# Optimization experiments

Hardware: AMD Instinct MI355X
Metric: run time of the kernel (lower is better)

Reference implementation:

```python
import jax, jax.numpy as jnp
import numpy as np

USER_NUM = 100000   # number of users
ITEM_NUM = 50000    # number of items
HIDDEN = 64         # embedding dim
B = 16384           # batch size
K = 50              # neighbors per item


def setup_inputs() -> dict:
    key = jax.random.key(0)
    ks = jax.random.split(key, 8)
    user = jax.random.randint(ks[0], (B,), 0, USER_NUM, dtype=jnp.int32)
    # item ids are offset by USER_NUM into the shared embedding table
    pos = USER_NUM + jax.random.randint(ks[1], (B,), 0, ITEM_NUM, dtype=jnp.int32)
    neg = USER_NUM + jax.random.randint(ks[2], (B,), 0, ITEM_NUM, dtype=jnp.int32)
    pos_beta = jax.random.uniform(ks[3], (B,), dtype=jnp.float32)
    neg_beta = jax.random.uniform(ks[4], (B,), dtype=jnp.float32)
    weights = jax.random.uniform(ks[5], (ITEM_NUM, K), dtype=jnp.float32)
    neighbor = jax.random.randint(ks[6], (ITEM_NUM, K), 0, USER_NUM, dtype=jnp.int32)
    embs = 0.02 * jax.random.normal(ks[7], (USER_NUM + ITEM_NUM, HIDDEN), dtype=jnp.float32)
    return {"user": user, "pos": pos, "neg": neg, "pos_beta": pos_beta,
            "neg_beta": neg_beta, "weights": weights, "neighbor": neighbor,
            "embs": embs}


def reference(user, pos, neg, pos_beta, neg_beta, weights, neighbor, embs):
    user_emb = embs[user]                      # [B, D]
    pos_emb = embs[pos]                        # [B, D]
    neg_emb = embs[neg]                        # [B, D]
    item_idx = pos - USER_NUM                  # [B]
    pos_neighbor = neighbor[item_idx]          # [B, K] user ids
    pos_weight = weights[item_idx]             # [B, K]
    pos_neighbor_emb = embs[pos_neighbor]      # [B, K, D]

    pos_logits = jnp.einsum('id,id->i', user_emb, pos_emb)            # [B]
    neg_logits = jnp.einsum('id,id->i', user_emb, neg_emb)            # [B]
    pos_nb_logits = jnp.einsum('id,ikd->ik', user_emb, pos_neighbor_emb)  # [B, K]

    # -log(sigmoid(x)) == -log_sigmoid(x), numerically stable
    log_sig_pos = jax.nn.log_sigmoid(pos_logits)
    log_sig_negneg = jax.nn.log_sigmoid(-neg_logits)

    LI = jnp.sum(-jax.nn.log_sigmoid(pos_nb_logits) * pos_weight)
    LO = -jnp.sum(log_sig_pos) - jnp.sum(log_sig_negneg)
    LC = -jnp.sum(log_sig_pos * pos_beta) - jnp.sum(log_sig_negneg * neg_beta)
    return LC + LO + 2.5 * LI
```

## Files before the change

kernel.cpp:

```cpp
#include <hip/hip_runtime.h>

#define USER_NUM 100000
#define ITEM_NUM 50000
#define HIDDEN   64
#define BATCH    16384
#define KNB      50

__device__ __forceinline__ float log_sigmoid(float x) {
    return fminf(x, 0.0f) - __logf(1.0f + __expf(-fabsf(x)));
}

__device__ __forceinline__ float dot4(float4 a, float4 b) {
    return a.x * b.x + a.y * b.y + a.z * b.z + a.w * b.w;
}

__device__ __forceinline__ float red16(float v) {
    v += __shfl_xor(v, 1);
    v += __shfl_xor(v, 2);
    v += __shfl_xor(v, 4);
    v += __shfl_xor(v, 8);
    return v;
}

__global__ __launch_bounds__(256) void ultragcn_main(
    const int*   __restrict__ user,
    const int*   __restrict__ pos,
    const int*   __restrict__ neg,
    const float* __restrict__ pos_beta,
    const float* __restrict__ neg_beta,
    const float* __restrict__ weights,
    const int*   __restrict__ neighbor,
    const float* __restrict__ embs,
    float*       __restrict__ partial)
{
    const int tid  = threadIdx.x;
    const int wave = tid >> 6;
    const int lane = tid & 63;
    const int i    = blockIdx.x * 4 + wave;

    const int g  = lane >> 4;
    const int gl = lane & 15;

    const int u = user[i];
    const int p = pos[i];
    const int n = neg[i];

    const float4* embs4 = (const float4*)embs;

    const float4 u4 = embs4[(long long)u * 16 + gl];
    const float4 p4 = embs4[(long long)p * 16 + gl];
    const float4 n4 = embs4[(long long)n * 16 + gl];

    const float pos_logit = red16(dot4(u4, p4));
    const float neg_logit = red16(dot4(u4, n4));

    const int item = p - USER_NUM;

    int   nbv = 0;
    float wv  = 0.0f;
    if (lane < KNB) {
        nbv = neighbor[item * KNB + lane];
        wv  = weights[item * KNB + lane];
    }

    float li = 0.0f;
#pragma unroll
    for (int t = 0; t < 13; ++t) {
        const int   k  = 4 * t + g;
        const int   nb = __shfl(nbv, k);
        const float w  = __shfl(wv,  k);
        const float4 e4 = embs4[(long long)nb * 16 + gl];
        const float d   = red16(dot4(u4, e4));
        li += -log_sigmoid(d) * w;
    }
    li += __shfl_xor(li, 16);
    li += __shfl_xor(li, 32);

    const float pb = pos_beta[i];
    const float nb = neg_beta[i];
    const float contrib = 2.5f * li
                        - (1.0f + pb) * log_sigmoid(pos_logit)
                        - (1.0f + nb) * log_sigmoid(-neg_logit);

    __shared__ float s[4];
    if (lane == 0) s[wave] = contrib;
    __syncthreads();
    if (tid == 0) {
        partial[blockIdx.x] = s[0] + s[1] + s[2] + s[3];
    }
}

__global__ __launch_bounds__(256) void ultragcn_reduce(
    const float* __restrict__ partial, float* __restrict__ out, int n)
{
    const int tid  = threadIdx.x;
    const int lane = tid & 63;
    const int wave = tid >> 6;

    float s = 0.0f;
    for (int idx = tid; idx < n; idx += 256) s += partial[idx];

    s += __shfl_xor(s, 1);
    s += __shfl_xor(s, 2);
    s += __shfl_xor(s, 4);
    s += __shfl_xor(s, 8);
    s += __shfl_xor(s, 16);
    s += __shfl_xor(s, 32);

    __shared__ float ws[4];
    if (lane == 0) ws[wave] = s;
    __syncthreads();
    if (tid == 0) out[0] = ws[0] + ws[1] + ws[2] + ws[3];
}

extern "C" void kernel_launch(void* const* d_in, const int* in_sizes, int n_in,
                              void* d_out, int out_size, void* d_ws, size_t ws_size,
                              hipStream_t stream)
{
    const int*   user     = (const int*)  d_in[0];
    const int*   pos      = (const int*)  d_in[1];
    const int*   neg      = (const int*)  d_in[2];
    const float* pos_beta = (const float*)d_in[3];
    const float* neg_beta = (const float*)d_in[4];
    const float* weights  = (const float*)d_in[5];
    const int*   neighbor = (const int*)  d_in[6];
    const float* embs     = (const float*)d_in[7];

    float* out     = (float*)d_out;
    float* partial = (float*)d_ws;

    const int nblocks = BATCH / 4;
    ultragcn_main<<<nblocks, 256, 0, stream>>>(
        user, pos, neg, pos_beta, neg_beta, weights, neighbor, embs, partial);
    ultragcn_reduce<<<1, 256, 0, stream>>>(partial, out, nblocks);
}
```

Before: 40.18 us.

## Bucket neighbor pairs by neighbor user to reuse neighbor embedding loads

Replaces the per-batch-row neighbor gather with a two-phase scheme. First, atomics scatter each (neighbor, user, weight) triple into per-neighbor buckets, with an overflow list. Then a harvest kernel loads each neighbor embedding once and dots it against the bucketed user embeddings. The aim is to make the large neighbor-embedding gather reuse-friendly, but it adds 819k atomics, a memset, bucket scatter traffic and an extra kernel launch. The user-embedding gathers are still random.

After: 107.6 us. +167.7%, slower.

```diff
diff --git a/kernel.cpp b/kernel.cpp
--- a/kernel.cpp
+++ b/kernel.cpp
@@ -5,13 +5,30 @@
 #define HIDDEN   64
 #define BATCH    16384
 #define KNB      50
+#define NPAIRS   (BATCH * KNB)
+#define CAP      16
+
+#define PAIR_BLOCKS  (NPAIRS / 256)
+#define LOCLC_BLOCKS (BATCH / 16)
+#define K3_ROWBLKS   (USER_NUM / 16)
+#define K3_OVFBLKS   256
+#define K3_BLOCKS    (K3_ROWBLKS + K3_OVFBLKS)
+
+#define OVF_CNT_OFF   0u
+#define COUNTS_OFF    256u
+#define BUCKETS_OFF   (1u << 19)
+#define OVERFLOW_OFF  (1u << 24)
+#define PARTIAL1_OFF  (1u << 25)
+#define PARTIAL2_OFF  ((1u << 25) + 8192u)
+
+typedef float  f4 __attribute__((ext_vector_type(4)));
 
 __device__ __forceinline__ float log_sigmoid(float x) {
     return fminf(x, 0.0f) - __logf(1.0f + __expf(-fabsf(x)));
 }
 
-__device__ __forceinline__ float dot4(float4 a, float4 b) {
-    return a.x * b.x + a.y * b.y + a.z * b.z + a.w * b.w;
+__device__ __forceinline__ float dot4(f4 a, f4 b) {
+    return a[0] * b[0] + a[1] * b[1] + a[2] * b[2] + a[3] * b[3];
 }
 
 __device__ __forceinline__ float red16(float v) {
@@ -22,7 +39,7 @@
     return v;
 }
 
-__global__ __launch_bounds__(256) void ultragcn_main(
+__global__ __launch_bounds__(256) void k_build(
     const int*   __restrict__ user,
     const int*   __restrict__ pos,
     const int*   __restrict__ neg,
@@ -31,74 +48,157 @@
     const float* __restrict__ weights,
     const int*   __restrict__ neighbor,
     const float* __restrict__ embs,
-    float*       __restrict__ partial)
-{
+    char*        __restrict__ ws)
+{
+    unsigned* counts   = (unsigned*)(ws + COUNTS_OFF);
+    unsigned* ovf_cnt  = (unsigned*)(ws + OVF_CNT_OFF);
+    uint2*    buckets  = (uint2*)   (ws + BUCKETS_OFF);
+    uint4*    overflow = (uint4*)   (ws + OVERFLOW_OFF);
+    float*    partial1 = (float*)   (ws + PARTIAL1_OFF);
+
+    const int bid = blockIdx.x;
+    if (bid < PAIR_BLOCKS) {
+        const int idx  = bid * 256 + threadIdx.x;
+        const int i    = idx / KNB;
+        const int k    = idx - i * KNB;
+        const int item = pos[i] - USER_NUM;
+        const int nb   = neighbor[item * KNB + k];
+        const float w  = weights[item * KNB + k];
+        const unsigned uid = (unsigned)user[i];
+        const unsigned slot = atomicAdd(&counts[nb], 1u);
+        if (slot < CAP) {
+            buckets[nb * CAP + slot] = make_uint2(uid, __float_as_uint(w));
+        } else {
+            const unsigned o = atomicAdd(ovf_cnt, 1u);
+            overflow[o] = make_uint4((unsigned)nb, uid, __float_as_uint(w), 0u);
+        }
+        return;
+    }
+
+    const int lbid = bid - PAIR_BLOCKS;
     const int tid  = threadIdx.x;
     const int wave = tid >> 6;
     const int lane = tid & 63;
-    const int i    = blockIdx.x * 4 + wave;
-
-    const int g  = lane >> 4;
-    const int gl = lane & 15;
+    const int g    = lane >> 4;
+    const int gl   = lane & 15;
+    const int i    = lbid * 16 + wave * 4 + g;
+
+    const char* eb = (const char*)embs;
+    const unsigned goff = (unsigned)(gl << 4);
 
     const int u = user[i];
     const int p = pos[i];
     const int n = neg[i];
 
-    const float4* embs4 = (const float4*)embs;
-
-    const float4 u4 = embs4[(long long)u * 16 + gl];
-    const float4 p4 = embs4[(long long)p * 16 + gl];
-    const float4 n4 = embs4[(long long)n * 16 + gl];
-
-    const float pos_logit = red16(dot4(u4, p4));
-    const float neg_logit = red16(dot4(u4, n4));
-
-    const int item = p - USER_NUM;
-
-    int   nbv = 0;
-    float wv  = 0.0f;
-    if (lane < KNB) {
-        nbv = neighbor[item * KNB + lane];
-        wv  = weights[item * KNB + lane];
-    }
-
-    float li = 0.0f;
-#pragma unroll
-    for (int t = 0; t < 13; ++t) {
-        const int   k  = 4 * t + g;
-        const int   nb = __shfl(nbv, k);
-        const float w  = __shfl(wv,  k);
-        const float4 e4 = embs4[(long long)nb * 16 + gl];
-        const float d   = red16(dot4(u4, e4));
-        li += -log_sigmoid(d) * w;
-    }
-    li += __shfl_xor(li, 16);
-    li += __shfl_xor(li, 32);
-
-    const float pb = pos_beta[i];
-    const float nb = neg_beta[i];
-    const float contrib = 2.5f * li
-                        - (1.0f + pb) * log_sigmoid(pos_logit)
-                        - (1.0f + nb) * log_sigmoid(-neg_logit);
+    const f4 u4 = *(const f4*)(eb + (unsigned)u * 256u + goff);
+    const f4 p4 = *(const f4*)(eb + (unsigned)p * 256u + goff);
+    const f4 n4 = *(const f4*)(eb + (unsigned)n * 256u + goff);
+
+    const float pl = red16(dot4(u4, p4));
+    const float nl = red16(dot4(u4, n4));
+
+    const float pb  = pos_beta[i];
+    const float nbt = neg_beta[i];
+    float contrib = -(1.0f + pb)  * log_sigmoid(pl)
+                  - (1.0f + nbt) * log_sigmoid(-nl);
+    contrib += __shfl_xor(contrib, 16);
+    contrib += __shfl_xor(contrib, 32);
 
     __shared__ float s[4];
     if (lane == 0) s[wave] = contrib;
     __syncthreads();
-    if (tid == 0) {
-        partial[blockIdx.x] = s[0] + s[1] + s[2] + s[3];
+    if (tid == 0) partial1[lbid] = s[0] + s[1] + s[2] + s[3];
+}
+
+__global__ __launch_bounds__(256) void k_harvest(
+    const int*   __restrict__ user,
+    const float* __restrict__ embs,
+    const char*  __restrict__ ws,
+    float*       __restrict__ partial2)
+{
+    const unsigned* counts   = (const unsigned*)(ws + COUNTS_OFF);
+    const unsigned* ovf_cnt  = (const unsigned*)(ws + OVF_CNT_OFF);
+    const uint2*    buckets  = (const uint2*)   (ws + BUCKETS_OFF);
+    const uint4*    overflow = (const uint4*)   (ws + OVERFLOW_OFF);
+
+    const int tid  = threadIdx.x;
+    const int wave = tid >> 6;
+    const int lane = tid & 63;
+    const int g    = lane >> 4;
+    const int gl   = lane & 15;
+    const unsigned goff = (unsigned)(gl << 4);
+    const int base = lane & 48;
+
+    const char* eb = (const char*)embs;
+    float acc = 0.0f;
+
+    if (blockIdx.x < K3_ROWBLKS) {
+        const int r = blockIdx.x * 16 + wave * 4 + g;
+        const unsigned cnt  = counts[r];
+        const unsigned cntC = cnt < CAP ? cnt : CAP;
+        const uint2 be = buckets[r * CAP + gl];
+
+        if (cntC) {
+            const f4 e4 = __builtin_nontemporal_load((const f4*)(eb + (unsigned)r * 256u + goff));
+            for (unsigned c = 0; c < cntC; c += 4) {
+                unsigned uidj[4]; float wj[4];
+#pragma unroll
+                for (int j = 0; j < 4; ++j) {
+                    const unsigned cc  = c + (unsigned)j;
+                    const int      src = base + (int)(cc & 15u);
+                    const unsigned uu  = (unsigned)__shfl((int)be.x, src);
+                    const unsigned wb  = (unsigned)__shfl((int)be.y, src);
+                    const bool     v   = cc < cntC;
+                    uidj[j] = v ? uu : 0u;
+                    wj[j]   = v ? __uint_as_float(wb) : 0.0f;
+                }
+                const f4 a0 = *(const f4*)(eb + uidj[0] * 256u + goff);
+                const f4 a1 = *(const f4*)(eb + uidj[1] * 256u + goff);
+                const f4 a2 = *(const f4*)(eb + uidj[2] * 256u + goff);
+                const f4 a3 = *(const f4*)(eb + uidj[3] * 256u + goff);
+                float d0 = red16(dot4(a0, e4));
+                float d1 = red16(dot4(a1, e4));
+                float d2 = red16(dot4(a2, e4));
+                float d3 = red16(dot4(a3, e4));
+                acc += wj[0] * (-log_sigmoid(d0));
+                acc += wj[1] * (-log_sigmoid(d1));
+                acc += wj[2] * (-log_sigmoid(d2));
+                acc += wj[3] * (-log_sigmoid(d3));
+            }
+        }
+    } else {
+        const unsigned total = *ovf_cnt;
+        const int ob   = blockIdx.x - K3_ROWBLKS;
+        const unsigned gidx = (unsigned)(ob * 16 + wave * 4 + g);
+        for (unsigned e = gidx; e < total; e += K3_OVFBLKS * 16u) {
+            const uint4 ov = overflow[e];
+            const f4 e4 = *(const f4*)(eb + ov.x * 256u + goff);
+            const f4 a4 = *(const f4*)(eb + ov.y * 256u + goff);
+            const float d = red16(dot4(a4, e4));
+            acc += __uint_as_float(ov.z) * (-log_sigmoid(d));
+        }
     }
-}
-
-__global__ __launch_bounds__(256) void ultragcn_reduce(
-    const float* __restrict__ partial, float* __restrict__ out, int n)
+
+    acc += __shfl_xor(acc, 16);
+    acc += __shfl_xor(acc, 32);
+    __shared__ float s[4];
+    if (lane == 0) s[wave] = acc;
+    __syncthreads();
+    if (tid == 0) partial2[blockIdx.x] = 2.5f * (s[0] + s[1] + s[2] + s[3]);
+}
+
+__global__ __launch_bounds__(256) void k_final(
+    const float* __restrict__ partial1,
+    const float* __restrict__ partial2,
+    float*       __restrict__ out)
 {
     const int tid  = threadIdx.x;
     const int lane = tid & 63;
     const int wave = tid >> 6;
 
     float s = 0.0f;
-    for (int idx = tid; idx < n; idx += 256) s += partial[idx];
+    for (int i = tid; i < LOCLC_BLOCKS; i += 256) s += partial1[i];
+    for (int i = tid; i < K3_BLOCKS;   i += 256) s += partial2[i];
 
     s += __shfl_xor(s, 1);
     s += __shfl_xor(s, 2);
@@ -107,10 +207,10 @@
     s += __shfl_xor(s, 16);
     s += __shfl_xor(s, 32);
 
-    __shared__ float ws[4];
-    if (lane == 0) ws[wave] = s;
+    __shared__ float ws_[4];
+    if (lane == 0) ws_[wave] = s;
     __syncthreads();
-    if (tid == 0) out[0] = ws[0] + ws[1] + ws[2] + ws[3];
+    if (tid == 0) out[0] = ws_[0] + ws_[1] + ws_[2] + ws_[3];
 }
 
 extern "C" void kernel_launch(void* const* d_in, const int* in_sizes, int n_in,
@@ -126,11 +226,17 @@
     const int*   neighbor = (const int*)  d_in[6];
     const float* embs     = (const float*)d_in[7];
 
-    float* out     = (float*)d_out;
-    float* partial = (float*)d_ws;
-
-    const int nblocks = BATCH / 4;
-    ultragcn_main<<<nblocks, 256, 0, stream>>>(
-        user, pos, neg, pos_beta, neg_beta, weights, neighbor, embs, partial);
-    ultragcn_reduce<<<1, 256, 0, stream>>>(partial, out, nblocks);
-}
+    char* ws = (char*)d_ws;
+
+    hipMemsetAsync(ws, 0, COUNTS_OFF + USER_NUM * sizeof(unsigned), stream);
+
+    k_build<<<PAIR_BLOCKS + LOCLC_BLOCKS, 256, 0, stream>>>(
+        user, pos, neg, pos_beta, neg_beta, weights, neighbor, embs, ws);
+
+    k_harvest<<<K3_BLOCKS, 256, 0, stream>>>(
+        user, embs, ws, (float*)(ws + PARTIAL2_OFF));
+
+    k_final<<<1, 256, 0, stream>>>(
+        (const float*)(ws + PARTIAL1_OFF), (const float*)(ws + PARTIAL2_OFF),
+        (float*)d_out);
+}
```
